# Kernel tuning notes

Hardware: AMD Instinct MI355X
Metric: run time of the kernel (lower is better)

Reference implementation:

```python
import jax, jax.numpy as jnp
import numpy as np

EPS = 1e-06  # used both as eps and as the F.threshold threshold (mqjs passes eps as th)


def _pair_log_dist_sum(x1, x2, th):
    # dist[i,j] = ||x1_i||^2 + ||x2_j||^2 - 2 x1_i . x2_j  (n x n)
    x1x2 = x1 @ x2.T
    sq1 = jnp.sum(x1 * x1, axis=1)[:, None]
    sq2 = jnp.sum(x2 * x2, axis=1)[None, :]
    dist = sq1 + sq2 - 2.0 * x1x2
    # F.threshold(dist, th, 1): values <= th -> 1; then clamp(min=1), sqrt, log, row-sum
    dist = jnp.where(dist > th, dist, 1.0)
    dist = jnp.maximum(dist, 1.0)
    return jnp.sum(0.5 * jnp.log(dist), axis=1)  # log(sqrt(d)) == 0.5*log(d)


def _mqjs(inp, tgt, eps):
    n = inp.shape[0]
    x1 = inp.reshape(n, -1)
    x2 = tgt.reshape(n, -1)
    p = (x1 + x2) / 2.0
    ce = _pair_log_dist_sum(x1, p, eps) + _pair_log_dist_sum(x2, p, eps)
    se = _pair_log_dist_sum(x1, x1, eps) * (n / (n - 1))
    return jnp.mean(ce - se)


def setup_inputs() -> dict:
    key = jax.random.key(0)
    k1, k2 = jax.random.split(key)
    n, d = 8192, 256
    inp = jax.random.normal(k1, (n, d), dtype=jnp.float32)
    tgt = jax.random.normal(k2, (n, d), dtype=jnp.float32)
    return {"input": inp, "target": tgt}


def reference(input, target):
    return _mqjs(input, target, EPS)
```

## Files before the change

kernel.cpp:

```cpp
#include <hip/hip_runtime.h>

#define N 8192
#define D 256
#define BM 128
#define BJ 64
#define JG 4
#define IG 4
#define GJP (N / (BJ * JG))
#define GIG (N / (BM * IG))
#define NPART (3 * GIG * GJP)

typedef int   i32x4 __attribute__((ext_vector_type(4)));
typedef int   i32x8 __attribute__((ext_vector_type(8)));
typedef float f32x4 __attribute__((ext_vector_type(4)));
typedef float f32x2 __attribute__((ext_vector_type(2)));

__device__ __forceinline__ unsigned pack_fp8x4(float a, float b, float c, float d) {
    unsigned lo = __builtin_amdgcn_cvt_pk_fp8_f32(a, b, 0, false);
    return __builtin_amdgcn_cvt_pk_fp8_f32(c, d, lo, true);
}
__device__ __forceinline__ float dequant_sumsq(unsigned q) {
    const float v0 = __builtin_amdgcn_cvt_f32_fp8(q, 0);
    const float v1 = __builtin_amdgcn_cvt_f32_fp8(q, 1);
    const float v2 = __builtin_amdgcn_cvt_f32_fp8(q, 2);
    const float v3 = __builtin_amdgcn_cvt_f32_fp8(q, 3);
    return fmaf(v0, v0, fmaf(v1, v1, fmaf(v2, v2, v3 * v3)));
}

__global__ void prep_kernel(const float* __restrict__ x1, const float* __restrict__ x2,
                            unsigned* __restrict__ x1q, unsigned* __restrict__ x2q,
                            unsigned* __restrict__ pq,
                            float* __restrict__ sq1, float* __restrict__ sq2,
                            float* __restrict__ sqp) {
    const int tid = threadIdx.x, lane = tid & 63, wv = tid >> 6;
    const int row = blockIdx.x * 4 + wv;
    const size_t eb = (size_t)row * D + lane * 4;
    const float4 a = *(const float4*)(x1 + eb);
    const float4 b = *(const float4*)(x2 + eb);
    const float px = 0.5f * (a.x + b.x), py = 0.5f * (a.y + b.y);
    const float pz = 0.5f * (a.z + b.z), pw = 0.5f * (a.w + b.w);
    const unsigned qa = pack_fp8x4(a.x, a.y, a.z, a.w);
    const unsigned qb = pack_fp8x4(b.x, b.y, b.z, b.w);
    const unsigned qp = pack_fp8x4(px, py, pz, pw);
    const size_t wb = (size_t)row * (D / 4) + lane;
    x1q[wb] = qa; x2q[wb] = qb; pq[wb] = qp;
    float s1 = dequant_sumsq(qa), s2 = dequant_sumsq(qb), sp = dequant_sumsq(qp);
    #pragma unroll
    for (int o = 32; o > 0; o >>= 1) {
        s1 += __shfl_down(s1, o, 64);
        s2 += __shfl_down(s2, o, 64);
        sp += __shfl_down(sp, o, 64);
    }
    if (lane == 0) { sq1[row] = s1; sq2[row] = s2; sqp[row] = sp; }
}

__device__ __forceinline__ f32x4 mfma8(i32x8 a, i32x8 b, f32x4 c) {
    return __builtin_amdgcn_mfma_scale_f32_16x16x128_f8f6f4(
        a, b, c, 0, 0, 0, 0x7F7F7F7F, 0, 0x7F7F7F7F);
}

__device__ __forceinline__ i32x8 frag_at(const unsigned char* b, int olo, int ohi) {
    const i32x4 lo = *(const i32x4*)(b + olo);
    const i32x4 hi = *(const i32x4*)(b + ohi);
    i32x8 f;
    f[0] = lo[0]; f[1] = lo[1]; f[2] = lo[2]; f[3] = lo[3];
    f[4] = hi[0]; f[5] = hi[1]; f[6] = hi[2]; f[7] = hi[3];
    return f;
}

__device__ __forceinline__ void stageB8(const unsigned char* __restrict__ g,
                                        unsigned char* s, int rowbase, size_t kb,
                                        int wv, int srow, int sblk) {
    const int row = wv * 8 + srow;
    __builtin_amdgcn_global_load_lds(
        (const __attribute__((address_space(1))) void*)(g + (size_t)(rowbase + row) * D + kb + sblk * 16),
        (__attribute__((address_space(3))) void*)(s + wv * 1024), 16, 0, 0);
}

__device__ __forceinline__ float logsumP(const f32x4 (&acc)[2][2],
                                         const f32x2 (&sa01)[2], const f32x2 (&sa23)[2],
                                         const float sb[2]) {
    float s = 0.0f;
    #pragma unroll
    for (int ti = 0; ti < 2; ++ti) {
        f32x2 pr = {1.0f, 1.0f};
        #pragma unroll
        for (int tj = 0; tj < 2; ++tj) {
            const f32x2 sbv = {sb[tj], sb[tj]};
            const f32x2 t01 = sa01[ti] + sbv, t23 = sa23[ti] + sbv;
            const f32x2 v01 = {acc[ti][tj][0], acc[ti][tj][1]};
            const f32x2 v23 = {acc[ti][tj][2], acc[ti][tj][3]};
            f32x2 d01 = t01 - 2.0f * v01;
            f32x2 d23 = t23 - 2.0f * v23;
            d01 = __builtin_elementwise_max(d01, (f32x2){1.0f, 1.0f});
            d23 = __builtin_elementwise_max(d23, (f32x2){1.0f, 1.0f});
            pr *= d01; pr *= d23;
        }
        s += __log2f(pr.x * pr.y);
    }
    return s;
}

__device__ __forceinline__ float logsumStraddle(const f32x4 (&acc)[2][2],
                                                const f32x2 (&sa01)[2], const f32x2 (&sa23)[2],
                                                const float sb[2],
                                                int wr, int wc, int quad, int l15,
                                                int I0, int J0) {
    float s = 0.0f;
    #pragma unroll
    for (int ti = 0; ti < 2; ++ti) {
        #pragma unroll
        for (int tj = 0; tj < 2; ++tj) {
            const int j = J0 + wc * 32 + tj * 16 + l15;
            float pr = 1.0f;
            #pragma unroll
            for (int r = 0; r < 4; ++r) {
                const int i = I0 + wr * 32 + ti * 16 + quad * 4 + r;
                const float sav = (r < 2) ? ((r & 1) ? sa01[ti].y : sa01[ti].x)
                                          : ((r & 1) ? sa23[ti].y : sa23[ti].x);
                float d = fmaf(-2.0f, acc[ti][tj][r], sav + sb[tj]);
                d = fmaxf(d, 1.0f);
                const float t = (j > i) ? d : 1.0f;
                const float u = (j >= i) ? d : 1.0f;
                pr *= t * u;
            }
            s += __log2f(pr);
        }
    }
    return s;
}

__device__ __forceinline__ void sgb_region() {
    __builtin_amdgcn_sched_group_barrier(0x020, 2, 0);
    __builtin_amdgcn_sched_group_barrier(0x100, 8, 0);
    #pragma unroll
    for (int i = 0; i < 8; ++i) {
        __builtin_amdgcn_sched_group_barrier(0x008, 1, 0);
        __builtin_amdgcn_sched_group_barrier(0x002, 6, 0);
    }
}

__global__ __launch_bounds__(512, 2) void mqjs_main(
    const unsigned char* __restrict__ x1q, const unsigned char* __restrict__ x2q,
    const unsigned char* __restrict__ pq,
    const float* __restrict__ sq1, const float* __restrict__ sq2,
    const float* __restrict__ sqp, float* __restrict__ partials) {

    __shared__ __align__(16) unsigned char Bs[JG * 16384];
    __shared__ float red[8];

    const int tid = threadIdx.x;
    const int lane = tid & 63;
    const int wv = tid >> 6;
    const int wr = wv >> 1, wc = wv & 1;
    const int quad = lane >> 4, l15 = lane & 15;
    const int srow = lane >> 3;
    const int sblk = (lane & 7) ^ srow;

    const int z = blockIdx.z;
    const int jbase = blockIdx.x * JG;
    const int Ibase = blockIdx.y * (BM * IG);
    const int pid = (z * GIG + blockIdx.y) * GJP + blockIdx.x;
    const float wse = -(float)N / (float)(N - 1);
    const int Jmax0 = (jbase + JG - 1) * BJ;

    if (z == 2 && Jmax0 < Ibase) {
        if (tid == 0) partials[pid] = 0.0f;
        return;
    }

    const unsigned char* Ag = (z == 1) ? x2q : x1q;
    const unsigned char* Bg = (z == 2) ? x1q : pq;
    const float* sqAg = (z == 1) ? sq2 : sq1;
    const float* sqBg = (z == 2) ? sq1 : sqp;

    #pragma unroll
    for (int jj = 0; jj < JG; ++jj) {
        stageB8(Bg, &Bs[jj * 16384],        (jbase + jj) * BJ, 0,   wv, srow, sblk);
        stageB8(Bg, &Bs[jj * 16384 + 8192], (jbase + jj) * BJ, 128, wv, srow, sblk);
    }

    asm volatile("s_waitcnt vmcnt(0)" ::: "memory");
    __syncthreads();

    const int m0 = wc * 32 + l15;
    const int r7 = m0 & 7;
    const int o0 = m0 * 128 + (((2 * quad)     ^ r7) << 4);
    const int o1 = m0 * 128 + (((2 * quad + 1) ^ r7) << 4);

    float tsum = 0.0f;
    const f32x4 zero4 = {0.0f, 0.0f, 0.0f, 0.0f};

    if (z < 2) {
        #pragma unroll 1
        for (int it = 0; it < IG; ++it) {
            const int I0 = Ibase + it * BM;

            i32x8 af[2][2];
            f32x2 sa01[2], sa23[2];
            #pragma unroll
            for (int ti = 0; ti < 2; ++ti) {
                #pragma unroll
                for (int kc = 0; kc < 2; ++kc) {
                    const size_t ro = (size_t)(I0 + wr * 32 + ti * 16 + l15) * D + kc * 128 + quad * 32;
                    af[kc][ti] = *(const i32x8*)(Ag + ro);
                }
                const int sbase = I0 + wr * 32 + ti * 16 + quad * 4;
                const float4 sv = *(const float4*)(sqAg + sbase);
                sa01[ti] = (f32x2){sv.x, sv.y};
                sa23[ti] = (f32x2){sv.z, sv.w};
            }

            auto TILE = [&](int jj, f32x4 (&acc)[2][2], float (&sb)[2]) {
                const unsigned char* tb = &Bs[jj * 16384];
                const float* sp = sqBg + (jbase + jj) * BJ + m0;
                sb[0] = sp[0]; sb[1] = sp[16];
                i32x8 b0 = frag_at(tb, o0, o1);
                i32x8 b1 = frag_at(tb + 2048, o0, o1);
                acc[0][0] = mfma8(af[0][0], b0, zero4);
                acc[0][1] = mfma8(af[0][0], b1, zero4);
                acc[1][0] = mfma8(af[0][1], b0, zero4);
                acc[1][1] = mfma8(af[0][1], b1, zero4);
                b0 = frag_at(tb + 8192, o0, o1);
                b1 = frag_at(tb + 8192 + 2048, o0, o1);
                acc[0][0] = mfma8(af[1][0], b0, acc[0][0]);
                acc[0][1] = mfma8(af[1][0], b1, acc[0][1]);
                acc[1][0] = mfma8(af[1][1], b0, acc[1][0]);
                acc[1][1] = mfma8(af[1][1], b1, acc[1][1]);
            };
            auto EPI = [&](const f32x4 (&acc)[2][2], const float (&sb)[2]) {
                tsum += 0.5f * logsumP(acc, sa01, sa23, sb);
            };

            f32x4 accA[2][2], accB[2][2];
            float sbA[2], sbB[2];
            TILE(0, accA, sbA);
            TILE(1, accB, sbB); EPI(accA, sbA); sgb_region();
            TILE(2, accA, sbA); EPI(accB, sbB); sgb_region();
            TILE(3, accB, sbB); EPI(accA, sbA); sgb_region();
            EPI(accB, sbB);
        }
    } else {
        #pragma unroll 1
        for (int it = 0; it < IG; ++it) {
            const int I0 = Ibase + it * BM;
            if (Jmax0 < I0) continue;

            i32x8 af[2][2];
            f32x2 sa01[2], sa23[2];
            #pragma unroll
            for (int ti = 0; ti < 2; ++ti) {
                #pragma unroll
                for (int kc = 0; kc < 2; ++kc) {
                    const size_t ro = (size_t)(I0 + wr * 32 + ti * 16 + l15) * D + kc * 128 + quad * 32;
                    af[kc][ti] = *(const i32x8*)(Ag + ro);
                }
                const int sbase = I0 + wr * 32 + ti * 16 + quad * 4;
                const float4 sv = *(const float4*)(sqAg + sbase);
                sa01[ti] = (f32x2){sv.x, sv.y};
                sa23[ti] = (f32x2){sv.z, sv.w};
            }

            #pragma unroll 1
            for (int jj = 0; jj < JG; ++jj) {
                const int J0 = (jbase + jj) * BJ;
                if (J0 < I0) continue;

                const unsigned char* tb = &Bs[jj * 16384];
                const float* sp = sqBg + J0 + m0;
                float sb[2];
                sb[0] = sp[0]; sb[1] = sp[16];

                f32x4 acc[2][2];
                __builtin_amdgcn_s_setprio(1);
                i32x8 b0 = frag_at(tb, o0, o1);
                i32x8 b1 = frag_at(tb + 2048, o0, o1);
                acc[0][0] = mfma8(af[0][0], b0, zero4);
                acc[0][1] = mfma8(af[0][0], b1, zero4);
                acc[1][0] = mfma8(af[0][1], b0, zero4);
                acc[1][1] = mfma8(af[0][1], b1, zero4);
                b0 = frag_at(tb + 8192, o0, o1);
                b1 = frag_at(tb + 8192 + 2048, o0, o1);
                acc[0][0] = mfma8(af[1][0], b0, acc[0][0]);
                acc[0][1] = mfma8(af[1][0], b1, acc[0][1]);
                acc[1][0] = mfma8(af[1][1], b0, acc[1][0]);
                acc[1][1] = mfma8(af[1][1], b1, acc[1][1]);
                __builtin_amdgcn_s_setprio(0);

                if (J0 >= I0 + BM) {
                    tsum += wse * logsumP(acc, sa01, sa23, sb);
                } else {
                    tsum += 0.5f * wse * logsumStraddle(acc, sa01, sa23, sb,
                                                        wr, wc, quad, l15, I0, J0);
                }
            }
        }
    }

    tsum *= 0.6931471805599453f;
    #pragma unroll
    for (int o = 32; o > 0; o >>= 1) tsum += __shfl_down(tsum, o, 64);
    if (lane == 0) red[wv] = tsum;
    __syncthreads();
    if (tid == 0) {
        float t = 0.0f;
        #pragma unroll
        for (int i = 0; i < 8; ++i) t += red[i];
        partials[pid] = t;
    }
}

__global__ void finalize_kernel(const float* __restrict__ partials, float* __restrict__ out) {
    const int tid = threadIdx.x;
    const float4 v = ((const float4*)partials)[tid];
    double s = (double)v.x + (double)v.y + (double)v.z + (double)v.w;
    #pragma unroll
    for (int o = 32; o > 0; o >>= 1) s += __shfl_down(s, o, 64);
    __shared__ double r[6];
    if ((tid & 63) == 0) r[tid >> 6] = s;
    __syncthreads();
    if (tid == 0) {
        double t = 0.0;
        #pragma unroll
        for (int i = 0; i < 6; ++i) t += r[i];
        out[0] = (float)(t / (double)N);
    }
}

extern "C" void kernel_launch(void* const* d_in, const int* in_sizes, int n_in,
                              void* d_out, int out_size, void* d_ws, size_t ws_size,
                              hipStream_t stream) {
    const float* x1 = (const float*)d_in[0];
    const float* x2 = (const float*)d_in[1];

    char* ws = (char*)d_ws;
    const size_t MBYTES = (size_t)N * D;
    unsigned* x1q = (unsigned*)(ws);
    unsigned* x2q = (unsigned*)(ws + MBYTES);
    unsigned* pq  = (unsigned*)(ws + 2 * MBYTES);
    float* sq1 = (float*)(ws + 3 * MBYTES);
    float* sq2 = (float*)(ws + 3 * MBYTES + (size_t)N * 4);
    float* sqp = (float*)(ws + 3 * MBYTES + (size_t)N * 8);
    float* partials = (float*)(ws + 3 * MBYTES + (size_t)N * 12);

    prep_kernel<<<N / 4, 256, 0, stream>>>(x1, x2, x1q, x2q, pq, sq1, sq2, sqp);
    mqjs_main<<<dim3(GJP, GIG, 3), 512, 0, stream>>>(
        (const unsigned char*)x1q, (const unsigned char*)x2q, (const unsigned char*)pq,
        sq1, sq2, sqp, partials);
    finalize_kernel<<<1, 384, 0, stream>>>(partials, (float*)d_out);
}
```

Before: 125.0 us.

## Fuse x1·p and x2·p cross-entropy passes to share staged p tiles

```diff
diff --git a/kernel.cpp b/kernel.cpp
--- a/kernel.cpp
+++ b/kernel.cpp
@@ -8,7 +8,7 @@
 #define IG 4
 #define GJP (N / (BJ * JG))
 #define GIG (N / (BM * IG))
-#define NPART (3 * GIG * GJP)
+#define NPART (2 * GIG * GJP)
 
 typedef int   i32x4 __attribute__((ext_vector_type(4)));
 typedef int   i32x8 __attribute__((ext_vector_type(8)));
@@ -130,13 +130,13 @@
     return s;
 }
 
-__device__ __forceinline__ void sgb_region() {
+__device__ __forceinline__ void sgb_fused() {
     __builtin_amdgcn_sched_group_barrier(0x020, 2, 0);
     __builtin_amdgcn_sched_group_barrier(0x100, 8, 0);
     #pragma unroll
-    for (int i = 0; i < 8; ++i) {
+    for (int i = 0; i < 16; ++i) {
         __builtin_amdgcn_sched_group_barrier(0x008, 1, 0);
-        __builtin_amdgcn_sched_group_barrier(0x002, 6, 0);
+        __builtin_amdgcn_sched_group_barrier(0x002, 8, 0);
     }
 }
 
@@ -164,15 +164,13 @@
     const float wse = -(float)N / (float)(N - 1);
     const int Jmax0 = (jbase + JG - 1) * BJ;
 
-    if (z == 2 && Jmax0 < Ibase) {
+    if (z == 1 && Jmax0 < Ibase) {
         if (tid == 0) partials[pid] = 0.0f;
         return;
     }
 
-    const unsigned char* Ag = (z == 1) ? x2q : x1q;
-    const unsigned char* Bg = (z == 2) ? x1q : pq;
-    const float* sqAg = (z == 1) ? sq2 : sq1;
-    const float* sqBg = (z == 2) ? sq1 : sqp;
+    const unsigned char* Bg = (z == 1) ? x1q : pq;
+    const float* sqBg = (z == 1) ? sq1 : sqp;
 
     #pragma unroll
     for (int jj = 0; jj < JG; ++jj) {
@@ -191,10 +189,74 @@
     float tsum = 0.0f;
     const f32x4 zero4 = {0.0f, 0.0f, 0.0f, 0.0f};
 
-    if (z < 2) {
+    if (z == 0) {
         #pragma unroll 1
         for (int it = 0; it < IG; ++it) {
             const int I0 = Ibase + it * BM;
+
+            i32x8 af1[2][2], af2[2][2];
+            f32x2 sa1_01[2], sa1_23[2], sa2_01[2], sa2_23[2];
+            #pragma unroll
+            for (int ti = 0; ti < 2; ++ti) {
+                #pragma unroll
+                for (int kc = 0; kc < 2; ++kc) {
+                    const size_t ro = (size_t)(I0 + wr * 32 + ti * 16 + l15) * D + kc * 128 + quad * 32;
+                    af1[kc][ti] = *(const i32x8*)(x1q + ro);
+                    af2[kc][ti] = *(const i32x8*)(x2q + ro);
+                }
+                const int sbase = I0 + wr * 32 + ti * 16 + quad * 4;
+                const float4 s1v = *(const float4*)(sq1 + sbase);
+                const float4 s2v = *(const float4*)(sq2 + sbase);
+                sa1_01[ti] = (f32x2){s1v.x, s1v.y};
+                sa1_23[ti] = (f32x2){s1v.z, s1v.w};
+                sa2_01[ti] = (f32x2){s2v.x, s2v.y};
+                sa2_23[ti] = (f32x2){s2v.z, s2v.w};
+            }
+
+            auto TILE2 = [&](int jj, f32x4 (&a1)[2][2], f32x4 (&a2)[2][2], float (&sb)[2]) {
+                const unsigned char* tb = &Bs[jj * 16384];
+                const float* sp = sqBg + (jbase + jj) * BJ + m0;
+                sb[0] = sp[0]; sb[1] = sp[16];
+                i32x8 b0 = frag_at(tb, o0, o1);
+                i32x8 b1 = frag_at(tb + 2048, o0, o1);
+                a1[0][0] = mfma8(af1[0][0], b0, zero4);
+                a2[0][0] = mfma8(af2[0][0], b0, zero4);
+                a1[0][1] = mfma8(af1[0][0], b1, zero4);
+                a2[0][1] = mfma8(af2[0][0], b1, zero4);
+                a1[1][0] = mfma8(af1[0][1], b0, zero4);
+                a2[1][0] = mfma8(af2[0][1], b0, zero4);
+                a1[1][1] = mfma8(af1[0][1], b1, zero4);
+                a2[1][1] = mfma8(af2[0][1], b1, zero4);
+                b0 = frag_at(tb + 8192, o0, o1);
+                b1 = frag_at(tb + 8192 + 2048, o0, o1);
+                a1[0][0] = mfma8(af1[1][0], b0, a1[0][0]);
+                a2[0][0] = mfma8(af2[1][0], b0, a2[0][0]);
+                a1[0][1] = mfma8(af1[1][0], b1, a1[0][1]);
+                a2[0][1] = mfma8(af2[1][0], b1, a2[0][1]);
+                a1[1][0] = mfma8(af1[1][1], b0, a1[1][0]);
+                a2[1][0] = mfma8(af2[1][1], b0, a2[1][0]);
+                a1[1][1] = mfma8(af1[1][1], b1, a1[1][1]);
+                a2[1][1] = mfma8(af2[1][1], b1, a2[1][1]);
+            };
+            auto EPI2 = [&](const f32x4 (&a1)[2][2], const f32x4 (&a2)[2][2],
+                            const float (&sb)[2]) {
+                tsum += 0.5f * (logsumP(a1, sa1_01, sa1_23, sb)
+                              + logsumP(a2, sa2_01, sa2_23, sb));
+            };
+
+            f32x4 aA1[2][2], aA2[2][2], aB1[2][2], aB2[2][2];
+            float sbA[2], sbB[2];
+            TILE2(0, aA1, aA2, sbA);
+            TILE2(1, aB1, aB2, sbB); EPI2(aA1, aA2, sbA); sgb_fused();
+            TILE2(2, aA1, aA2, sbA); EPI2(aB1, aB2, sbB); sgb_fused();
+            TILE2(3, aB1, aB2, sbB); EPI2(aA1, aA2, sbA); sgb_fused();
+            EPI2(aB1, aB2, sbB);
+        }
+    } else {
+        #pragma unroll 1
+        for (int it = 0; it < IG; ++it) {
+            const int I0 = Ibase + it * BM;
+            if (Jmax0 < I0) continue;
 
             i32x8 af[2][2];
             f32x2 sa01[2], sa23[2];
@@ -203,60 +265,10 @@
                 #pragma unroll
                 for (int kc = 0; kc < 2; ++kc) {
                     const size_t ro = (size_t)(I0 + wr * 32 + ti * 16 + l15) * D + kc * 128 + quad * 32;
-                    af[kc][ti] = *(const i32x8*)(Ag + ro);
+                    af[kc][ti] = *(const i32x8*)(x1q + ro);
                 }
                 const int sbase = I0 + wr * 32 + ti * 16 + quad * 4;
-                const float4 sv = *(const float4*)(sqAg + sbase);
-                sa01[ti] = (f32x2){sv.x, sv.y};
-                sa23[ti] = (f32x2){sv.z, sv.w};
-            }
-
-            auto TILE = [&](int jj, f32x4 (&acc)[2][2], float (&sb)[2]) {
-                const unsigned char* tb = &Bs[jj * 16384];
-                const float* sp = sqBg + (jbase + jj) * BJ + m0;
-                sb[0] = sp[0]; sb[1] = sp[16];
-                i32x8 b0 = frag_at(tb, o0, o1);
-                i32x8 b1 = frag_at(tb + 2048, o0, o1);
-                acc[0][0] = mfma8(af[0][0], b0, zero4);
-                acc[0][1] = mfma8(af[0][0], b1, zero4);
-                acc[1][0] = mfma8(af[0][1], b0, zero4);
-                acc[1][1] = mfma8(af[0][1], b1, zero4);
-                b0 = frag_at(tb + 8192, o0, o1);
-                b1 = frag_at(tb + 8192 + 2048, o0, o1);
-                acc[0][0] = mfma8(af[1][0], b0, acc[0][0]);
-                acc[0][1] = mfma8(af[1][0], b1, acc[0][1]);
-                acc[1][0] = mfma8(af[1][1], b0, acc[1][0]);
-                acc[1][1] = mfma8(af[1][1], b1, acc[1][1]);
-            };
-            auto EPI = [&](const f32x4 (&acc)[2][2], const float (&sb)[2]) {
-                tsum += 0.5f * logsumP(acc, sa01, sa23, sb);
-            };
-
-            f32x4 accA[2][2], accB[2][2];
-            float sbA[2], sbB[2];
-            TILE(0, accA, sbA);
-            TILE(1, accB, sbB); EPI(accA, sbA); sgb_region();
-            TILE(2, accA, sbA); EPI(accB, sbB); sgb_region();
-            TILE(3, accB, sbB); EPI(accA, sbA); sgb_region();
-            EPI(accB, sbB);
-        }
-    } else {
-        #pragma unroll 1
-        for (int it = 0; it < IG; ++it) {
-            const int I0 = Ibase + it * BM;
-            if (Jmax0 < I0) continue;
-
-            i32x8 af[2][2];
-            f32x2 sa01[2], sa23[2];
-            #pragma unroll
-            for (int ti = 0; ti < 2; ++ti) {
-                #pragma unroll
-                for (int kc = 0; kc < 2; ++kc) {
-                    const size_t ro = (size_t)(I0 + wr * 32 + ti * 16 + l15) * D + kc * 128 + quad * 32;
-                    af[kc][ti] = *(const i32x8*)(Ag + ro);
-                }
-                const int sbase = I0 + wr * 32 + ti * 16 + quad * 4;
-                const float4 sv = *(const float4*)(sqAg + sbase);
+                const float4 sv = *(const float4*)(sq1 + sbase);
                 sa01[ti] = (f32x2){sv.x, sv.y};
                 sa23[ti] = (f32x2){sv.z, sv.w};
             }
@@ -316,13 +328,13 @@
     double s = (double)v.x + (double)v.y + (double)v.z + (double)v.w;
     #pragma unroll
     for (int o = 32; o > 0; o >>= 1) s += __shfl_down(s, o, 64);
-    __shared__ double r[6];
+    __shared__ double r[4];
     if ((tid & 63) == 0) r[tid >> 6] = s;
     __syncthreads();
     if (tid == 0) {
         double t = 0.0;
         #pragma unroll
-        for (int i = 0; i < 6; ++i) t += r[i];
+        for (int i = 0; i < 4; ++i) t += r[i];
         out[0] = (float)(t / (double)N);
     }
 }
@@ -344,8 +356,8 @@
     float* partials = (float*)(ws + 3 * MBYTES + (size_t)N * 12);
 
     prep_kernel<<<N / 4, 256, 0, stream>>>(x1, x2, x1q, x2q, pq, sq1, sq2, sqp);
-    mqjs_main<<<dim3(GJP, GIG, 3), 512, 0, stream>>>(
+    mqjs_main<<<dim3(GJP, GIG, 2), 512, 0, stream>>>(
         (const unsigned char*)x1q, (const unsigned char*)x2q, (const unsigned char*)pq,
         sq1, sq2, sqp, partials);
-    finalize_kernel<<<1, 384, 0, stream>>>(partials, (float*)d_out);
-}
+    finalize_kernel<<<1, 256, 0, stream>>>(partials, (float*)d_out);
+}
```

Measured after the change: 134.1 us. 1.07x slower.

## Split each 128x64 tile across 16 waves with one 16-column subtile per wave

Applied to the files above, without the earlier changes.

```diff
diff --git a/kernel.cpp b/kernel.cpp
--- a/kernel.cpp
+++ b/kernel.cpp
@@ -68,91 +68,86 @@
     return f;
 }
 
-__device__ __forceinline__ void stageB8(const unsigned char* __restrict__ g,
-                                        unsigned char* s, int rowbase, size_t kb,
-                                        int wv, int srow, int sblk) {
-    const int row = wv * 8 + srow;
+__device__ __forceinline__ void stageB16(const unsigned char* __restrict__ g,
+                                         unsigned char* s, int rowbase,
+                                         int wv, int srow, int sblk) {
+    const int chunk = wv >> 3;
+    const int grp = wv & 7;
+    const int row = grp * 8 + srow;
     __builtin_amdgcn_global_load_lds(
-        (const __attribute__((address_space(1))) void*)(g + (size_t)(rowbase + row) * D + kb + sblk * 16),
-        (__attribute__((address_space(3))) void*)(s + wv * 1024), 16, 0, 0);
-}
-
-__device__ __forceinline__ float logsumP(const f32x4 (&acc)[2][2],
+        (const __attribute__((address_space(1))) void*)(g + (size_t)(rowbase + row) * D + chunk * 128 + sblk * 16),
+        (__attribute__((address_space(3))) void*)(s + chunk * 8192 + grp * 1024), 16, 0, 0);
+}
+
+__device__ __forceinline__ float logsumP(const f32x4 (&acc)[2],
                                          const f32x2 (&sa01)[2], const f32x2 (&sa23)[2],
-                                         const float sb[2]) {
+                                         const float sb) {
     float s = 0.0f;
+    const f32x2 sbv = {sb, sb};
     #pragma unroll
     for (int ti = 0; ti < 2; ++ti) {
-        f32x2 pr = {1.0f, 1.0f};
-        #pragma unroll
-        for (int tj = 0; tj < 2; ++tj) {
-            const f32x2 sbv = {sb[tj], sb[tj]};
-            const f32x2 t01 = sa01[ti] + sbv, t23 = sa23[ti] + sbv;
-            const f32x2 v01 = {acc[ti][tj][0], acc[ti][tj][1]};
-            const f32x2 v23 = {acc[ti][tj][2], acc[ti][tj][3]};
-            f32x2 d01 = t01 - 2.0f * v01;
-            f32x2 d23 = t23 - 2.0f * v23;
-            d01 = __builtin_elementwise_max(d01, (f32x2){1.0f, 1.0f});
-            d23 = __builtin_elementwise_max(d23, (f32x2){1.0f, 1.0f});
-            pr *= d01; pr *= d23;
-        }
+        const f32x2 t01 = sa01[ti] + sbv, t23 = sa23[ti] + sbv;
+        const f32x2 v01 = {acc[ti][0], acc[ti][1]};
+        const f32x2 v23 = {acc[ti][2], acc[ti][3]};
+        f32x2 d01 = t01 - 2.0f * v01;
+        f32x2 d23 = t23 - 2.0f * v23;
+        d01 = __builtin_elementwise_max(d01, (f32x2){1.0f, 1.0f});
+        d23 = __builtin_elementwise_max(d23, (f32x2){1.0f, 1.0f});
+        const f32x2 pr = d01 * d23;
         s += __log2f(pr.x * pr.y);
     }
     return s;
 }
 
-__device__ __forceinline__ float logsumStraddle(const f32x4 (&acc)[2][2],
+__device__ __forceinline__ float logsumStraddle(const f32x4 (&acc)[2],
                                                 const f32x2 (&sa01)[2], const f32x2 (&sa23)[2],
-                                                const float sb[2],
+                                                const float sb,
                                                 int wr, int wc, int quad, int l15,
                                                 int I0, int J0) {
     float s = 0.0f;
+    const int j = J0 + wc * 16 + l15;
     #pragma unroll
     for (int ti = 0; ti < 2; ++ti) {
+        float pr = 1.0f;
         #pragma unroll
-        for (int tj = 0; tj < 2; ++tj) {
-            const int j = J0 + wc * 32 + tj * 16 + l15;
-            float pr = 1.0f;
-            #pragma unroll
-            for (int r = 0; r < 4; ++r) {
-                const int i = I0 + wr * 32 + ti * 16 + quad * 4 + r;
-                const float sav = (r < 2) ? ((r & 1) ? sa01[ti].y : sa01[ti].x)
-                                          : ((r & 1) ? sa23[ti].y : sa23[ti].x);
-                float d = fmaf(-2.0f, acc[ti][tj][r], sav + sb[tj]);
-                d = fmaxf(d, 1.0f);
-                const float t = (j > i) ? d : 1.0f;
-                const float u = (j >= i) ? d : 1.0f;
-                pr *= t * u;
-            }
-            s += __log2f(pr);
+        for (int r = 0; r < 4; ++r) {
+            const int i = I0 + wr * 32 + ti * 16 + quad * 4 + r;
+            const float sav = (r < 2) ? ((r & 1) ? sa01[ti].y : sa01[ti].x)
+                                      : ((r & 1) ? sa23[ti].y : sa23[ti].x);
+            float d = fmaf(-2.0f, acc[ti][r], sav + sb);
+            d = fmaxf(d, 1.0f);
+            const float t = (j > i) ? d : 1.0f;
+            const float u = (j >= i) ? d : 1.0f;
+            pr *= t * u;
         }
+        s += __log2f(pr);
     }
     return s;
 }
 
 __device__ __forceinline__ void sgb_region() {
-    __builtin_amdgcn_sched_group_barrier(0x020, 2, 0);
-    __builtin_amdgcn_sched_group_barrier(0x100, 8, 0);
-    #pragma unroll
-    for (int i = 0; i < 8; ++i) {
+    __builtin_amdgcn_sched_group_barrier(0x020, 1, 0);
+    __builtin_amdgcn_sched_group_barrier(0x100, 4, 0);
+    #pragma unroll
+    for (int i = 0; i < 4; ++i) {
         __builtin_amdgcn_sched_group_barrier(0x008, 1, 0);
         __builtin_amdgcn_sched_group_barrier(0x002, 6, 0);
     }
 }
 
-__global__ __launch_bounds__(512, 2) void mqjs_main(
+__global__ __launch_bounds__(1024, 2) void mqjs_main(
     const unsigned char* __restrict__ x1q, const unsigned char* __restrict__ x2q,
     const unsigned char* __restrict__ pq,
     const float* __restrict__ sq1, const float* __restrict__ sq2,
     const float* __restrict__ sqp, float* __restrict__ partials) {
 
     __shared__ __align__(16) unsigned char Bs[JG * 16384];
-    __shared__ float red[8];
+    __shared__ float red[16];
 
     const int tid = threadIdx.x;
     const int lane = tid & 63;
     const int wv = tid >> 6;
-    const int wr = wv >> 1, wc = wv & 1;
+    const int wr = wv >> 2, wc = wv & 3;
     const int quad = lane >> 4, l15 = lane & 15;
     const int srow = lane >> 3;
     const int sblk = (lane & 7) ^ srow;
@@ -175,15 +170,13 @@
     const float* sqBg = (z == 2) ? sq1 : sqp;
 
     #pragma unroll
-    for (int jj = 0; jj < JG; ++jj) {
-        stageB8(Bg, &Bs[jj * 16384],        (jbase + jj) * BJ, 0,   wv, srow, sblk);
-        stageB8(Bg, &Bs[jj * 16384 + 8192], (jbase + jj) * BJ, 128, wv, srow, sblk);
-    }
+    for (int jj = 0; jj < JG; ++jj)
+        stageB16(Bg, &Bs[jj * 16384], (jbase + jj) * BJ, wv, srow, sblk);
 
     asm volatile("s_waitcnt vmcnt(0)" ::: "memory");
     __syncthreads();
 
-    const int m0 = wc * 32 + l15;
+    const int m0 = wc * 16 + l15;
     const int r7 = m0 & 7;
     const int o0 = m0 * 128 + (((2 * quad)     ^ r7) << 4);
     const int o1 = m0 * 128 + (((2 * quad + 1) ^ r7) << 4);
@@ -211,29 +204,22 @@
                 sa23[ti] = (f32x2){sv.z, sv.w};
             }
 
-            auto TILE = [&](int jj, f32x4 (&acc)[2][2], float (&sb)[2]) {
+            auto TILE = [&](int jj, f32x4 (&acc)[2], float &sb) {
                 const unsigned char* tb = &Bs[jj * 16384];
-                const float* sp = sqBg + (jbase + jj) * BJ + m0;
-                sb[0] = sp[0]; sb[1] = sp[16];
+                sb = sqBg[(jbase + jj) * BJ + m0];
                 i32x8 b0 = frag_at(tb, o0, o1);
-                i32x8 b1 = frag_at(tb + 2048, o0, o1);
-                acc[0][0] = mfma8(af[0][0], b0, zero4);
-                acc[0][1] = mfma8(af[0][0], b1, zero4);
-                acc[1][0] = mfma8(af[0][1], b0, zero4);
-                acc[1][1] = mfma8(af[0][1], b1, zero4);
+                acc[0] = mfma8(af[0][0], b0, zero4);
+                acc[1] = mfma8(af[0][1], b0, zero4);
                 b0 = frag_at(tb + 8192, o0, o1);
-                b1 = frag_at(tb + 8192 + 2048, o0, o1);
-                acc[0][0] = mfma8(af[1][0], b0, acc[0][0]);
-                acc[0][1] = mfma8(af[1][0], b1, acc[0][1]);
-                acc[1][0] = mfma8(af[1][1], b0, acc[1][0]);
-                acc[1][1] = mfma8(af[1][1], b1, acc[1][1]);
+                acc[0] = mfma8(af[1][0], b0, acc[0]);
+                acc[1] = mfma8(af[1][1], b0, acc[1]);
             };
-            auto EPI = [&](const f32x4 (&acc)[2][2], const float (&sb)[2]) {
+            auto EPI = [&](const f32x4 (&acc)[2], float sb) {
                 tsum += 0.5f * logsumP(acc, sa01, sa23, sb);
             };
 
-            f32x4 accA[2][2], accB[2][2];
-            float sbA[2], sbB[2];
+            f32x4 accA[2], accB[2];
+            float sbA, sbB;
             TILE(0, accA, sbA);
             TILE(1, accB, sbB); EPI(accA, sbA); sgb_region();
             TILE(2, accA, sbA); EPI(accB, sbB); sgb_region();
@@ -267,24 +253,16 @@
                 if (J0 < I0) continue;
 
                 const unsigned char* tb = &Bs[jj * 16384];
-                const float* sp = sqBg + J0 + m0;
-                float sb[2];
-                sb[0] = sp[0]; sb[1] = sp[16];
-
-                f32x4 acc[2][2];
+                float sb = sqBg[J0 + m0];
+
+                f32x4 acc[2];
                 __builtin_amdgcn_s_setprio(1);
                 i32x8 b0 = frag_at(tb, o0, o1);
-                i32x8 b1 = frag_at(tb + 2048, o0, o1);
-                acc[0][0] = mfma8(af[0][0], b0, zero4);
-                acc[0][1] = mfma8(af[0][0], b1, zero4);
-                acc[1][0] = mfma8(af[0][1], b0, zero4);
-                acc[1][1] = mfma8(af[0][1], b1, zero4);
+                acc[0] = mfma8(af[0][0], b0, zero4);
+                acc[1] = mfma8(af[0][1], b0, zero4);
                 b0 = frag_at(tb + 8192, o0, o1);
-                b1 = frag_at(tb + 8192 + 2048, o0, o1);
-                acc[0][0] = mfma8(af[1][0], b0, acc[0][0]);
-                acc[0][1] = mfma8(af[1][0], b1, acc[0][1]);
-                acc[1][0] = mfma8(af[1][1], b0, acc[1][0]);
-                acc[1][1] = mfma8(af[1][1], b1, acc[1][1]);
+                acc[0] = mfma8(af[1][0], b0, acc[0]);
+                acc[1] = mfma8(af[1][1], b0, acc[1]);
                 __builtin_amdgcn_s_setprio(0);
 
                 if (J0 >= I0 + BM) {
@@ -305,7 +283,7 @@
     if (tid == 0) {
         float t = 0.0f;
         #pragma unroll
-        for (int i = 0; i < 8; ++i) t += red[i];
+        for (int i = 0; i < 16; ++i) t += red[i];
         partials[pid] = t;
     }
 }
@@ -344,7 +322,7 @@
     float* partials = (float*)(ws + 3 * MBYTES + (size_t)N * 12);
 
     prep_kernel<<<N / 4, 256, 0, stream>>>(x1, x2, x1q, x2q, pq, sq1, sq2, sqp);
-    mqjs_main<<<dim3(GJP, GIG, 3), 512, 0, stream>>>(
+    mqjs_main<<<dim3(GJP, GIG, 3), 1024, 0, stream>>>(
         (const unsigned char*)x1q, (const unsigned char*)x2q, (const unsigned char*)pq,
         sq1, sq2, sqp, partials);
     finalize_kernel<<<1, 384, 0, stream>>>(partials, (float*)d_out);
```

After: 178.7 us. 43.0% more time.
